# Performance work log

Hardware: AMD Instinct MI355X
Metric: run time of the kernel (lower is better)

The kernel has to match this reference:

```python
import jax, jax.numpy as jnp
import numpy as np

B, H, S, D = 2, 16, 2048, 64
DILATION_RATE = 2

def dilated_global_mask(seq_len: int, dilation_rate: int) -> jnp.ndarray:
    # mask[i, j] = 1 if |i - j| % dilation_rate == 0 else 0  -> [S, S] float32
    i = jnp.arange(seq_len)[:, None]
    j = jnp.arange(seq_len)[None, :]
    return ((jnp.abs(i - j) % dilation_rate) == 0).astype(jnp.float32)

def setup_inputs() -> dict:
    key = jax.random.key(0)
    kq, kk, kv = jax.random.split(key, 3)
    queries = jax.random.normal(kq, (B, H, S, D), dtype=jnp.float32)
    keys = jax.random.normal(kk, (B, H, S, D), dtype=jnp.float32)
    values = jax.random.normal(kv, (B, H, S, D), dtype=jnp.float32)
    return {"queries": queries, "keys": keys, "values": values}

def reference(queries, keys, values):
    depth = queries.shape[-1]
    # scores: [B, H, S, S]
    scores = jnp.einsum("bhqd,bhkd->bhqk", queries, keys)
    scores = scores / jnp.sqrt(jnp.asarray(depth, dtype=jnp.float32))
    gmask = dilated_global_mask(keys.shape[-2], DILATION_RATE)  # [S, S]
    # NOTE: multiplicative masking (masked scores become 0, not -inf), as in source
    masked_scores = scores * gmask
    attention_probs = jax.nn.softmax(masked_scores, axis=-1)
    # dropout is identity at inference (training=None)
    out = jnp.einsum("bhqk,bhkd->bhqd", attention_probs, values)
    return out
```

## Files before the change

### kernel.cpp

```cpp
#include <hip/hip_runtime.h>
#include <hip/hip_bf16.h>


#define B_   2
#define H_   16
#define S_   2048
#define D_   64
#define SP_  1024
#define BQ   128
#define BK   64
#define NKT  (SP_ / BK)
#define NW   4

#define QSCALE 0.180336884f

#if __has_builtin(__builtin_amdgcn_exp2f)
#define EXP2(x) __builtin_amdgcn_exp2f(x)
#else
#define EXP2(x) exp2f(x)
#endif

typedef __bf16 bf16x8 __attribute__((ext_vector_type(8)));
typedef __bf16 bf16x4 __attribute__((ext_vector_type(4)));
typedef float  f32x4  __attribute__((ext_vector_type(4)));
typedef short  s16x4  __attribute__((ext_vector_type(4)));

static __device__ __forceinline__ f32x4 mfma16(bf16x4 a, bf16x4 b, f32x4 c) {
    return __builtin_amdgcn_mfma_f32_16x16x16bf16_1k(
        __builtin_bit_cast(s16x4, a), __builtin_bit_cast(s16x4, b), c, 0, 0, 0);
}

#define KSW(r, c8) ((((c8) ^ ((r) & 7)) << 3))

__global__ __launch_bounds__(256, 2) void attn_kernel(const float* __restrict__ Q,
                                                      const float* __restrict__ K,
                                                      const float* __restrict__ V,
                                                      float* __restrict__ out) {
    const int bh  = blockIdx.x;
    const int par = blockIdx.y;
    const int qt  = blockIdx.z;
    const int tid  = threadIdx.x;
    const int lane = tid & 63;
    const int wave = tid >> 6;
    const int l15  = lane & 15;
    const int quad = lane >> 4;

    __shared__ __align__(16) char arena[33792];
    __bf16 (*kbuf)[BK][64] = (__bf16 (*)[BK][64])arena;
    __bf16 (*vbuf)[D_][64] = (__bf16 (*)[D_][64])(arena + 16384);
    float  (*vred)[64]     = (float  (*)[64])(arena + 32768);

    const size_t base = (size_t)bh * S_ * D_;
    const float* Qb = Q + base;
    const float* Kb = K + base;
    const float* Vb = V + base;
    const int vofs = (par == 0) ? D_ : -D_;

    bf16x8 qf[2][2];
    #pragma unroll
    for (int qt2 = 0; qt2 < 2; ++qt2) {
        const int qrow = qt * BQ + wave * 32 + qt2 * 16 + l15;
        const float* qsrc = Qb + (size_t)(par + 2 * qrow) * D_ + quad * 8;
        #pragma unroll
        for (int ks = 0; ks < 2; ++ks) {
            const float4 a = *(const float4*)(qsrc + ks * 32);
            const float4 b = *(const float4*)(qsrc + ks * 32 + 4);
            bf16x8 w;
            w[0] = (__bf16)(a.x * QSCALE); w[1] = (__bf16)(a.y * QSCALE);
            w[2] = (__bf16)(a.z * QSCALE); w[3] = (__bf16)(a.w * QSCALE);
            w[4] = (__bf16)(b.x * QSCALE); w[5] = (__bf16)(b.y * QSCALE);
            w[6] = (__bf16)(b.z * QSCALE); w[7] = (__bf16)(b.w * QSCALE);
            qf[qt2][ks] = w;
        }
    }

    const int kr0 = tid >> 3;
    const int kc8 = tid & 7;

    float4 pka[2], pkb[2];
    float  pv[16], pvo[16];

    auto issue_loads = [&](int kt) {
        #pragma unroll
        for (int i = 0; i < 2; ++i) {
            const int r = i * 32 + kr0;
            const float* ksrc = Kb + (size_t)(par + 2 * (kt * BK + r)) * D_ + kc8 * 8;
            pka[i] = *(const float4*)ksrc;
            pkb[i] = *(const float4*)(ksrc + 4);
        }
        #pragma unroll
        for (int i = 0; i < 2; ++i) {
            const int c = wave + 4 * i;
            const float* vsrc = Vb + (size_t)(par + 2 * (kt * BK + c * 8)) * D_ + lane;
            #pragma unroll
            for (int j = 0; j < 8; ++j) {
                pv [i * 8 + j] = vsrc[(size_t)(2 * j) * D_];
                pvo[i * 8 + j] = vsrc[(size_t)(2 * j) * D_ + vofs];
            }
        }
    };

    float vo = 0.f;
    auto stage = [&](int buf) {
        #pragma unroll
        for (int i = 0; i < 2; ++i) {
            const int r = i * 32 + kr0;
            bf16x8 w;
            w[0] = (__bf16)pka[i].x; w[1] = (__bf16)pka[i].y;
            w[2] = (__bf16)pka[i].z; w[3] = (__bf16)pka[i].w;
            w[4] = (__bf16)pkb[i].x; w[5] = (__bf16)pkb[i].y;
            w[6] = (__bf16)pkb[i].z; w[7] = (__bf16)pkb[i].w;
            *(bf16x8*)&kbuf[buf][r][KSW(r, kc8)] = w;
        }
        #pragma unroll
        for (int i = 0; i < 2; ++i) {
            const int c = wave + 4 * i;
            bf16x8 w;
            #pragma unroll
            for (int j = 0; j < 8; ++j) w[j] = (__bf16)pv[i * 8 + j];
            *(bf16x8*)&vbuf[buf][lane][KSW(lane, c)] = w;
            vo += ((pvo[i*8+0] + pvo[i*8+1]) + (pvo[i*8+2] + pvo[i*8+3]))
                + ((pvo[i*8+4] + pvo[i*8+5]) + (pvo[i*8+6] + pvo[i*8+7]));
        }
    };

    issue_loads(0);
    stage(0);
    __syncthreads();

    f32x4 acc[2][4];
    #pragma unroll
    for (int q2 = 0; q2 < 2; ++q2)
        #pragma unroll
        for (int dt = 0; dt < 4; ++dt) acc[q2][dt] = (f32x4){0.f, 0.f, 0.f, 0.f};
    float l_acc[2] = {0.f, 0.f};

    for (int kt = 0; kt < NKT; ++kt) {
        const int cur = kt & 1;
        const bool pf = (kt + 1 < NKT);

        if (pf) issue_loads(kt + 1);

        const __bf16 (*kb)[64] = kbuf[cur];
        const __bf16 (*vb)[64] = vbuf[cur];

        bf16x8 ka[2][4];
        #pragma unroll
        for (int ks = 0; ks < 2; ++ks)
            #pragma unroll
            for (int kt4 = 0; kt4 < 4; ++kt4) {
                const int R = kt4 * 16 + l15;
                ka[ks][kt4] = *(const bf16x8*)&kb[R][KSW(R, ks * 4 + quad)];
            }
        bf16x4 va[4][4];
        #pragma unroll
        for (int dt = 0; dt < 4; ++dt) {
            const int R = dt * 16 + l15;
            const int ro = R & 7;
            #pragma unroll
            for (int kt4 = 0; kt4 < 4; ++kt4) {
                const int ch = (kt4 * 2 + (quad >> 1)) ^ ro;
                va[kt4][dt] = *(const bf16x4*)&vb[R][ch * 8 + (quad & 1) * 4];
            }
        }

        #pragma unroll
        for (int qt2 = 0; qt2 < 2; ++qt2) {
            f32x4 st[4];
            #pragma unroll
            for (int kt4 = 0; kt4 < 4; ++kt4) st[kt4] = (f32x4){0.f, 0.f, 0.f, 0.f};
            #pragma unroll
            for (int ks = 0; ks < 2; ++ks)
                #pragma unroll
                for (int kt4 = 0; kt4 < 4; ++kt4)
                    st[kt4] = __builtin_amdgcn_mfma_f32_16x16x32_bf16(
                        ka[ks][kt4], qf[qt2][ks], st[kt4], 0, 0, 0);
            #pragma unroll
            for (int kt4 = 0; kt4 < 4; ++kt4) {
                const float p0 = EXP2(st[kt4][0]);
                const float p1 = EXP2(st[kt4][1]);
                const float p2 = EXP2(st[kt4][2]);
                const float p3 = EXP2(st[kt4][3]);
                l_acc[qt2] += (p0 + p1) + (p2 + p3);
                bf16x4 pb;
                pb[0] = (__bf16)p0; pb[1] = (__bf16)p1;
                pb[2] = (__bf16)p2; pb[3] = (__bf16)p3;
                #pragma unroll
                for (int dt = 0; dt < 4; ++dt)
                    acc[qt2][dt] = mfma16(va[kt4][dt], pb, acc[qt2][dt]);
            }
        }

        if (pf) stage(1 - cur);
        __syncthreads();
    }

    vred[wave][lane] = vo;
    __syncthreads();

    f32x4 vs4[4];
    #pragma unroll
    for (int dt = 0; dt < 4; ++dt) {
        f32x4 s = (f32x4){0.f, 0.f, 0.f, 0.f};
        #pragma unroll
        for (int w = 0; w < NW; ++w)
            s += *(const f32x4*)&vred[w][dt * 16 + quad * 4];
        vs4[dt] = s;
    }
    float rz[2];
    #pragma unroll
    for (int qt2 = 0; qt2 < 2; ++qt2) {
        float Z = l_acc[qt2];
        Z += __shfl_xor(Z, 16);
        Z += __shfl_xor(Z, 32);
        rz[qt2] = 1.0f / (Z + 1024.0f);
    }

    float* tw = (float*)arena + wave * (16 * 68);
    #pragma unroll
    for (int qt2 = 0; qt2 < 2; ++qt2) {
        #pragma unroll
        for (int dt = 0; dt < 4; ++dt) {
            const f32x4 o = (acc[qt2][dt] + vs4[dt]) * rz[qt2];
            *(f32x4*)&tw[l15 * 68 + dt * 16 + quad * 4] = o;
        }
        #pragma unroll
        for (int i = 0; i < 4; ++i) {
            const int q = i * 4 + quad;
            const f32x4 ov = *(const f32x4*)&tw[q * 68 + l15 * 4];
            const int qg = par + 2 * (qt * BQ + wave * 32 + qt2 * 16 + q);
            *(f32x4*)&out[base + (size_t)qg * D_ + l15 * 4] = ov;
        }
    }
}

extern "C" void kernel_launch(void* const* d_in, const int* in_sizes, int n_in,
                              void* d_out, int out_size, void* d_ws, size_t ws_size,
                              hipStream_t stream) {
    const float* Q = (const float*)d_in[0];
    const float* K = (const float*)d_in[1];
    const float* V = (const float*)d_in[2];
    float* out = (float*)d_out;
    attn_kernel<<<dim3(B_ * H_, 2, SP_ / BQ), dim3(256), 0, stream>>>(Q, K, V, out);
}
```

Measured before the change: 112.3 us.

## Split each key tile across two wave groups with LDS reduction of partial outputs

```diff
diff --git a/kernel.cpp b/kernel.cpp
--- a/kernel.cpp
+++ b/kernel.cpp
@@ -10,7 +10,7 @@
 #define BQ   128
 #define BK   64
 #define NKT  (SP_ / BK)
-#define NW   4
+#define NW   8
 
 #define QSCALE 0.180336884f
 
@@ -32,7 +32,7 @@
 
 #define KSW(r, c8) ((((c8) ^ ((r) & 7)) << 3))
 
-__global__ __launch_bounds__(256, 2) void attn_kernel(const float* __restrict__ Q,
+__global__ __launch_bounds__(512, 4) void attn_kernel(const float* __restrict__ Q,
                                                       const float* __restrict__ K,
                                                       const float* __restrict__ V,
                                                       float* __restrict__ out) {
@@ -42,13 +42,17 @@
     const int tid  = threadIdx.x;
     const int lane = tid & 63;
     const int wave = tid >> 6;
+    const int w4   = wave & 3;
+    const int hk   = wave >> 2;
+    const int kt4b = hk * 2;
     const int l15  = lane & 15;
     const int quad = lane >> 4;
 
-    __shared__ __align__(16) char arena[33792];
+    __shared__ __align__(16) char arena[54272];
     __bf16 (*kbuf)[BK][64] = (__bf16 (*)[BK][64])arena;
     __bf16 (*vbuf)[D_][64] = (__bf16 (*)[D_][64])(arena + 16384);
     float  (*vred)[64]     = (float  (*)[64])(arena + 32768);
+    float  (*lred)[2][64]  = (float  (*)[2][64])(arena + 34816);
 
     const size_t base = (size_t)bh * S_ * D_;
     const float* Qb = Q + base;
@@ -59,7 +63,7 @@
     bf16x8 qf[2][2];
     #pragma unroll
     for (int qt2 = 0; qt2 < 2; ++qt2) {
-        const int qrow = qt * BQ + wave * 32 + qt2 * 16 + l15;
+        const int qrow = qt * BQ + w4 * 32 + qt2 * 16 + l15;
         const float* qsrc = Qb + (size_t)(par + 2 * qrow) * D_ + quad * 8;
         #pragma unroll
         for (int ks = 0; ks < 2; ++ks) {
@@ -76,52 +80,37 @@
 
     const int kr0 = tid >> 3;
     const int kc8 = tid & 7;
-
-    float4 pka[2], pkb[2];
-    float  pv[16], pvo[16];
+    const int vc  = wave;
+
+    float4 pka, pkb;
+    float  pv[8], pvo[8];
 
     auto issue_loads = [&](int kt) {
-        #pragma unroll
-        for (int i = 0; i < 2; ++i) {
-            const int r = i * 32 + kr0;
-            const float* ksrc = Kb + (size_t)(par + 2 * (kt * BK + r)) * D_ + kc8 * 8;
-            pka[i] = *(const float4*)ksrc;
-            pkb[i] = *(const float4*)(ksrc + 4);
-        }
-        #pragma unroll
-        for (int i = 0; i < 2; ++i) {
-            const int c = wave + 4 * i;
-            const float* vsrc = Vb + (size_t)(par + 2 * (kt * BK + c * 8)) * D_ + lane;
-            #pragma unroll
-            for (int j = 0; j < 8; ++j) {
-                pv [i * 8 + j] = vsrc[(size_t)(2 * j) * D_];
-                pvo[i * 8 + j] = vsrc[(size_t)(2 * j) * D_ + vofs];
-            }
+        const float* ksrc = Kb + (size_t)(par + 2 * (kt * BK + kr0)) * D_ + kc8 * 8;
+        pka = *(const float4*)ksrc;
+        pkb = *(const float4*)(ksrc + 4);
+        const float* vsrc = Vb + (size_t)(par + 2 * (kt * BK + vc * 8)) * D_ + lane;
+        #pragma unroll
+        for (int j = 0; j < 8; ++j) {
+            pv [j] = vsrc[(size_t)(2 * j) * D_];
+            pvo[j] = vsrc[(size_t)(2 * j) * D_ + vofs];
         }
     };
 
     float vo = 0.f;
     auto stage = [&](int buf) {
-        #pragma unroll
-        for (int i = 0; i < 2; ++i) {
-            const int r = i * 32 + kr0;
-            bf16x8 w;
-            w[0] = (__bf16)pka[i].x; w[1] = (__bf16)pka[i].y;
-            w[2] = (__bf16)pka[i].z; w[3] = (__bf16)pka[i].w;
-            w[4] = (__bf16)pkb[i].x; w[5] = (__bf16)pkb[i].y;
-            w[6] = (__bf16)pkb[i].z; w[7] = (__bf16)pkb[i].w;
-            *(bf16x8*)&kbuf[buf][r][KSW(r, kc8)] = w;
-        }
-        #pragma unroll
-        for (int i = 0; i < 2; ++i) {
-            const int c = wave + 4 * i;
-            bf16x8 w;
-            #pragma unroll
-            for (int j = 0; j < 8; ++j) w[j] = (__bf16)pv[i * 8 + j];
-            *(bf16x8*)&vbuf[buf][lane][KSW(lane, c)] = w;
-            vo += ((pvo[i*8+0] + pvo[i*8+1]) + (pvo[i*8+2] + pvo[i*8+3]))
-                + ((pvo[i*8+4] + pvo[i*8+5]) + (pvo[i*8+6] + pvo[i*8+7]));
-        }
+        bf16x8 w;
+        w[0] = (__bf16)pka.x; w[1] = (__bf16)pka.y;
+        w[2] = (__bf16)pka.z; w[3] = (__bf16)pka.w;
+        w[4] = (__bf16)pkb.x; w[5] = (__bf16)pkb.y;
+        w[6] = (__bf16)pkb.z; w[7] = (__bf16)pkb.w;
+        *(bf16x8*)&kbuf[buf][kr0][KSW(kr0, kc8)] = w;
+        bf16x8 wv;
+        #pragma unroll
+        for (int j = 0; j < 8; ++j) wv[j] = (__bf16)pv[j];
+        *(bf16x8*)&vbuf[buf][lane][KSW(lane, vc)] = wv;
+        vo += ((pvo[0] + pvo[1]) + (pvo[2] + pvo[3]))
+            + ((pvo[4] + pvo[5]) + (pvo[6] + pvo[7]));
     };
 
     issue_loads(0);
@@ -144,50 +133,50 @@
         const __bf16 (*kb)[64] = kbuf[cur];
         const __bf16 (*vb)[64] = vbuf[cur];
 
-        bf16x8 ka[2][4];
+        bf16x8 ka[2][2];
         #pragma unroll
         for (int ks = 0; ks < 2; ++ks)
             #pragma unroll
-            for (int kt4 = 0; kt4 < 4; ++kt4) {
-                const int R = kt4 * 16 + l15;
-                ka[ks][kt4] = *(const bf16x8*)&kb[R][KSW(R, ks * 4 + quad)];
+            for (int t = 0; t < 2; ++t) {
+                const int R = (kt4b + t) * 16 + l15;
+                ka[ks][t] = *(const bf16x8*)&kb[R][KSW(R, ks * 4 + quad)];
             }
-        bf16x4 va[4][4];
+        bf16x4 va[2][4];
         #pragma unroll
         for (int dt = 0; dt < 4; ++dt) {
             const int R = dt * 16 + l15;
             const int ro = R & 7;
             #pragma unroll
-            for (int kt4 = 0; kt4 < 4; ++kt4) {
-                const int ch = (kt4 * 2 + (quad >> 1)) ^ ro;
-                va[kt4][dt] = *(const bf16x4*)&vb[R][ch * 8 + (quad & 1) * 4];
+            for (int t = 0; t < 2; ++t) {
+                const int ch = ((kt4b + t) * 2 + (quad >> 1)) ^ ro;
+                va[t][dt] = *(const bf16x4*)&vb[R][ch * 8 + (quad & 1) * 4];
             }
         }
 
         #pragma unroll
         for (int qt2 = 0; qt2 < 2; ++qt2) {
-            f32x4 st[4];
-            #pragma unroll
-            for (int kt4 = 0; kt4 < 4; ++kt4) st[kt4] = (f32x4){0.f, 0.f, 0.f, 0.f};
+            f32x4 st[2];
+            #pragma unroll
+            for (int t = 0; t < 2; ++t) st[t] = (f32x4){0.f, 0.f, 0.f, 0.f};
             #pragma unroll
             for (int ks = 0; ks < 2; ++ks)
                 #pragma unroll
-                for (int kt4 = 0; kt4 < 4; ++kt4)
-                    st[kt4] = __builtin_amdgcn_mfma_f32_16x16x32_bf16(
-                        ka[ks][kt4], qf[qt2][ks], st[kt4], 0, 0, 0);
-            #pragma unroll
-            for (int kt4 = 0; kt4 < 4; ++kt4) {
-                const float p0 = EXP2(st[kt4][0]);
-                const float p1 = EXP2(st[kt4][1]);
-                const float p2 = EXP2(st[kt4][2]);
-                const float p3 = EXP2(st[kt4][3]);
+                for (int t = 0; t < 2; ++t)
+                    st[t] = __builtin_amdgcn_mfma_f32_16x16x32_bf16(
+                        ka[ks][t], qf[qt2][ks], st[t], 0, 0, 0);
+            #pragma unroll
+            for (int t = 0; t < 2; ++t) {
+                const float p0 = EXP2(st[t][0]);
+                const float p1 = EXP2(st[t][1]);
+                const float p2 = EXP2(st[t][2]);
+                const float p3 = EXP2(st[t][3]);
                 l_acc[qt2] += (p0 + p1) + (p2 + p3);
                 bf16x4 pb;
                 pb[0] = (__bf16)p0; pb[1] = (__bf16)p1;
                 pb[2] = (__bf16)p2; pb[3] = (__bf16)p3;
                 #pragma unroll
                 for (int dt = 0; dt < 4; ++dt)
-                    acc[qt2][dt] = mfma16(va[kt4][dt], pb, acc[qt2][dt]);
+                    acc[qt2][dt] = mfma16(va[t][dt], pb, acc[qt2][dt]);
             }
         }
 
@@ -196,39 +185,59 @@
     }
 
     vred[wave][lane] = vo;
-    __syncthreads();
-
-    f32x4 vs4[4];
-    #pragma unroll
-    for (int dt = 0; dt < 4; ++dt) {
-        f32x4 s = (f32x4){0.f, 0.f, 0.f, 0.f};
-        #pragma unroll
-        for (int w = 0; w < NW; ++w)
-            s += *(const f32x4*)&vred[w][dt * 16 + quad * 4];
-        vs4[dt] = s;
-    }
-    float rz[2];
+
+    float lf[2];
     #pragma unroll
     for (int qt2 = 0; qt2 < 2; ++qt2) {
         float Z = l_acc[qt2];
         Z += __shfl_xor(Z, 16);
         Z += __shfl_xor(Z, 32);
-        rz[qt2] = 1.0f / (Z + 1024.0f);
-    }
-
-    float* tw = (float*)arena + wave * (16 * 68);
+        lf[qt2] = Z;
+    }
+
+    if (hk) {
+        f32x4* ad = (f32x4*)(arena + (size_t)w4 * 8192);
+        #pragma unroll
+        for (int qt2 = 0; qt2 < 2; ++qt2) {
+            lred[w4][qt2][lane] = lf[qt2];
+            #pragma unroll
+            for (int dt = 0; dt < 4; ++dt)
+                ad[(qt2 * 4 + dt) * 64 + lane] = acc[qt2][dt];
+        }
+    }
+    __syncthreads();
+    if (hk) return;
+
+    f32x4 vs4[4];
+    #pragma unroll
+    for (int dt = 0; dt < 4; ++dt) {
+        f32x4 s = (f32x4){0.f, 0.f, 0.f, 0.f};
+        #pragma unroll
+        for (int w = 0; w < NW; ++w)
+            s += *(const f32x4*)&vred[w][dt * 16 + quad * 4];
+        vs4[dt] = s;
+    }
+    float rz[2];
+    #pragma unroll
+    for (int qt2 = 0; qt2 < 2; ++qt2)
+        rz[qt2] = 1.0f / (lf[qt2] + lred[w4][qt2][lane] + 1024.0f);
+
+    const f32x4* ad = (const f32x4*)(arena + (size_t)w4 * 8192);
+
+    float* tw = (float*)(arena + 36864) + w4 * (16 * 68);
     #pragma unroll
     for (int qt2 = 0; qt2 < 2; ++qt2) {
         #pragma unroll
         for (int dt = 0; dt < 4; ++dt) {
-            const f32x4 o = (acc[qt2][dt] + vs4[dt]) * rz[qt2];
+            const f32x4 o = (acc[qt2][dt] + ad[(qt2 * 4 + dt) * 64 + lane] + vs4[dt])
+                          * rz[qt2];
             *(f32x4*)&tw[l15 * 68 + dt * 16 + quad * 4] = o;
         }
         #pragma unroll
         for (int i = 0; i < 4; ++i) {
             const int q = i * 4 + quad;
             const f32x4 ov = *(const f32x4*)&tw[q * 68 + l15 * 4];
-            const int qg = par + 2 * (qt * BQ + wave * 32 + qt2 * 16 + q);
+            const int qg = par + 2 * (qt * BQ + w4 * 32 + qt2 * 16 + q);
             *(f32x4*)&out[base + (size_t)qg * D_ + l15 * 4] = ov;
         }
     }
@@ -241,5 +250,5 @@
     const float* K = (const float*)d_in[1];
     const float* V = (const float*)d_in[2];
     float* out = (float*)d_out;
-    attn_kernel<<<dim3(B_ * H_, 2, SP_ / BQ), dim3(256), 0, stream>>>(Q, K, V, out);
+    attn_kernel<<<dim3(B_ * H_, 2, SP_ / BQ), dim3(512), 0, stream>>>(Q, K, V, out);
 }
```

Measured after the change: 119.6 us. 6.5% more time.

## Precompute off-parity V column sums in a separate kernel and halve query tile

Applied to the files above, without the earlier changes.

```diff
diff --git a/kernel.cpp b/kernel.cpp
--- a/kernel.cpp
+++ b/kernel.cpp
@@ -7,10 +7,9 @@
 #define S_   2048
 #define D_   64
 #define SP_  1024
-#define BQ   128
+#define BQ   64
 #define BK   64
 #define NKT  (SP_ / BK)
-#define NW   4
 
 #define QSCALE 0.180336884f
 
@@ -32,9 +31,32 @@
 
 #define KSW(r, c8) ((((c8) ^ ((r) & 7)) << 3))
 
-__global__ __launch_bounds__(256, 2) void attn_kernel(const float* __restrict__ Q,
+__global__ __launch_bounds__(1024) void vsum_kernel(const float* __restrict__ V,
+                                                    float* __restrict__ vs) {
+    const int bp  = blockIdx.x;
+    const int bh  = bp >> 1;
+    const int par = bp & 1;
+    const int d   = threadIdx.x & 63;
+    const int rg  = threadIdx.x >> 6;
+    const float* Vb = V + (size_t)bh * S_ * D_;
+    float s = 0.f;
+    for (int r = rg; r < SP_; r += 16)
+        s += Vb[(size_t)(par + 2 * r) * D_ + d];
+    __shared__ float red[16][64];
+    red[rg][d] = s;
+    __syncthreads();
+    if (rg == 0) {
+        float t = 0.f;
+        #pragma unroll
+        for (int i = 0; i < 16; ++i) t += red[i][d];
+        vs[(size_t)bp * 64 + d] = t;
+    }
+}
+
+__global__ __launch_bounds__(256, 4) void attn_kernel(const float* __restrict__ Q,
                                                       const float* __restrict__ K,
                                                       const float* __restrict__ V,
+                                                      const float* __restrict__ vs,
                                                       float* __restrict__ out) {
     const int bh  = blockIdx.x;
     const int par = blockIdx.y;
@@ -45,21 +67,18 @@
     const int l15  = lane & 15;
     const int quad = lane >> 4;
 
-    __shared__ __align__(16) char arena[33792];
+    __shared__ __align__(16) char arena[32768];
     __bf16 (*kbuf)[BK][64] = (__bf16 (*)[BK][64])arena;
     __bf16 (*vbuf)[D_][64] = (__bf16 (*)[D_][64])(arena + 16384);
-    float  (*vred)[64]     = (float  (*)[64])(arena + 32768);
 
     const size_t base = (size_t)bh * S_ * D_;
     const float* Qb = Q + base;
     const float* Kb = K + base;
     const float* Vb = V + base;
-    const int vofs = (par == 0) ? D_ : -D_;
-
-    bf16x8 qf[2][2];
-    #pragma unroll
-    for (int qt2 = 0; qt2 < 2; ++qt2) {
-        const int qrow = qt * BQ + wave * 32 + qt2 * 16 + l15;
+
+    bf16x8 qf[2];
+    {
+        const int qrow = qt * BQ + wave * 16 + l15;
         const float* qsrc = Qb + (size_t)(par + 2 * qrow) * D_ + quad * 8;
         #pragma unroll
         for (int ks = 0; ks < 2; ++ks) {
@@ -70,7 +89,7 @@
             w[2] = (__bf16)(a.z * QSCALE); w[3] = (__bf16)(a.w * QSCALE);
             w[4] = (__bf16)(b.x * QSCALE); w[5] = (__bf16)(b.y * QSCALE);
             w[6] = (__bf16)(b.z * QSCALE); w[7] = (__bf16)(b.w * QSCALE);
-            qf[qt2][ks] = w;
+            qf[ks] = w;
         }
     }
 
@@ -78,7 +97,7 @@
     const int kc8 = tid & 7;
 
     float4 pka[2], pkb[2];
-    float  pv[16], pvo[16];
+    float  pv[16];
 
     auto issue_loads = [&](int kt) {
         #pragma unroll
@@ -93,14 +112,11 @@
             const int c = wave + 4 * i;
             const float* vsrc = Vb + (size_t)(par + 2 * (kt * BK + c * 8)) * D_ + lane;
             #pragma unroll
-            for (int j = 0; j < 8; ++j) {
-                pv [i * 8 + j] = vsrc[(size_t)(2 * j) * D_];
-                pvo[i * 8 + j] = vsrc[(size_t)(2 * j) * D_ + vofs];
-            }
+            for (int j = 0; j < 8; ++j)
+                pv[i * 8 + j] = vsrc[(size_t)(2 * j) * D_];
         }
     };
 
-    float vo = 0.f;
     auto stage = [&](int buf) {
         #pragma unroll
         for (int i = 0; i < 2; ++i) {
@@ -119,8 +135,6 @@
             #pragma unroll
             for (int j = 0; j < 8; ++j) w[j] = (__bf16)pv[i * 8 + j];
             *(bf16x8*)&vbuf[buf][lane][KSW(lane, c)] = w;
-            vo += ((pvo[i*8+0] + pvo[i*8+1]) + (pvo[i*8+2] + pvo[i*8+3]))
-                + ((pvo[i*8+4] + pvo[i*8+5]) + (pvo[i*8+6] + pvo[i*8+7]));
         }
     };
 
@@ -128,12 +142,10 @@
     stage(0);
     __syncthreads();
 
-    f32x4 acc[2][4];
+    f32x4 acc[4];
     #pragma unroll
-    for (int q2 = 0; q2 < 2; ++q2)
-        #pragma unroll
-        for (int dt = 0; dt < 4; ++dt) acc[q2][dt] = (f32x4){0.f, 0.f, 0.f, 0.f};
-    float l_acc[2] = {0.f, 0.f};
+    for (int dt = 0; dt < 4; ++dt) acc[dt] = (f32x4){0.f, 0.f, 0.f, 0.f};
+    float l_acc = 0.f;
 
     for (int kt = 0; kt < NKT; ++kt) {
         const int cur = kt & 1;
@@ -164,73 +176,54 @@
             }
         }
 
-        #pragma unroll
-        for (int qt2 = 0; qt2 < 2; ++qt2) {
-            f32x4 st[4];
-            #pragma unroll
-            for (int kt4 = 0; kt4 < 4; ++kt4) st[kt4] = (f32x4){0.f, 0.f, 0.f, 0.f};
-            #pragma unroll
-            for (int ks = 0; ks < 2; ++ks)
-                #pragma unroll
-                for (int kt4 = 0; kt4 < 4; ++kt4)
-                    st[kt4] = __builtin_amdgcn_mfma_f32_16x16x32_bf16(
-                        ka[ks][kt4], qf[qt2][ks], st[kt4], 0, 0, 0);
-            #pragma unroll
-            for (int kt4 = 0; kt4 < 4; ++kt4) {
-                const float p0 = EXP2(st[kt4][0]);
-                const float p1 = EXP2(st[kt4][1]);
-                const float p2 = EXP2(st[kt4][2]);
-                const float p3 = EXP2(st[kt4][3]);
-                l_acc[qt2] += (p0 + p1) + (p2 + p3);
-                bf16x4 pb;
-                pb[0] = (__bf16)p0; pb[1] = (__bf16)p1;
-                pb[2] = (__bf16)p2; pb[3] = (__bf16)p3;
-                #pragma unroll
-                for (int dt = 0; dt < 4; ++dt)
-                    acc[qt2][dt] = mfma16(va[kt4][dt], pb, acc[qt2][dt]);
-            }
+        f32x4 st[4];
+        #pragma unroll
+        for (int kt4 = 0; kt4 < 4; ++kt4) st[kt4] = (f32x4){0.f, 0.f, 0.f, 0.f};
+        #pragma unroll
+        for (int ks = 0; ks < 2; ++ks)
+            #pragma unroll
+            for (int kt4 = 0; kt4 < 4; ++kt4)
+                st[kt4] = __builtin_amdgcn_mfma_f32_16x16x32_bf16(
+                    ka[ks][kt4], qf[ks], st[kt4], 0, 0, 0);
+        #pragma unroll
+        for (int kt4 = 0; kt4 < 4; ++kt4) {
+            const float p0 = EXP2(st[kt4][0]);
+            const float p1 = EXP2(st[kt4][1]);
+            const float p2 = EXP2(st[kt4][2]);
+            const float p3 = EXP2(st[kt4][3]);
+            l_acc += (p0 + p1) + (p2 + p3);
+            bf16x4 pb;
+            pb[0] = (__bf16)p0; pb[1] = (__bf16)p1;
+            pb[2] = (__bf16)p2; pb[3] = (__bf16)p3;
+            #pragma unroll
+            for (int dt = 0; dt < 4; ++dt)
+                acc[dt] = mfma16(va[kt4][dt], pb, acc[dt]);
         }
 
         if (pf) stage(1 - cur);
         __syncthreads();
     }
 
-    vred[wave][lane] = vo;
-    __syncthreads();
-
-    f32x4 vs4[4];
+    float Z = l_acc;
+    Z += __shfl_xor(Z, 16);
+    Z += __shfl_xor(Z, 32);
+    const float rz = 1.0f / (Z + 1024.0f);
+
+    const float* vso = vs + ((size_t)(bh * 2 + (1 - par))) * 64;
+
+    float* tw = (float*)arena + wave * (16 * 68);
     #pragma unroll
     for (int dt = 0; dt < 4; ++dt) {
-        f32x4 s = (f32x4){0.f, 0.f, 0.f, 0.f};
-        #pragma unroll
-        for (int w = 0; w < NW; ++w)
-            s += *(const f32x4*)&vred[w][dt * 16 + quad * 4];
-        vs4[dt] = s;
-    }
-    float rz[2];
+        const f32x4 vs4 = *(const f32x4*)&vso[dt * 16 + quad * 4];
+        const f32x4 o = (acc[dt] + vs4) * rz;
+        *(f32x4*)&tw[l15 * 68 + dt * 16 + quad * 4] = o;
+    }
     #pragma unroll
-    for (int qt2 = 0; qt2 < 2; ++qt2) {
-        float Z = l_acc[qt2];
-        Z += __shfl_xor(Z, 16);
-        Z += __shfl_xor(Z, 32);
-        rz[qt2] = 1.0f / (Z + 1024.0f);
-    }
-
-    float* tw = (float*)arena + wave * (16 * 68);
-    #pragma unroll
-    for (int qt2 = 0; qt2 < 2; ++qt2) {
-        #pragma unroll
-        for (int dt = 0; dt < 4; ++dt) {
-            const f32x4 o = (acc[qt2][dt] + vs4[dt]) * rz[qt2];
-            *(f32x4*)&tw[l15 * 68 + dt * 16 + quad * 4] = o;
-        }
-        #pragma unroll
-        for (int i = 0; i < 4; ++i) {
-            const int q = i * 4 + quad;
-            const f32x4 ov = *(const f32x4*)&tw[q * 68 + l15 * 4];
-            const int qg = par + 2 * (qt * BQ + wave * 32 + qt2 * 16 + q);
-            *(f32x4*)&out[base + (size_t)qg * D_ + l15 * 4] = ov;
-        }
+    for (int i = 0; i < 4; ++i) {
+        const int q = i * 4 + quad;
+        const f32x4 ov = *(const f32x4*)&tw[q * 68 + l15 * 4];
+        const int qg = par + 2 * (qt * BQ + wave * 16 + q);
+        *(f32x4*)&out[base + (size_t)qg * D_ + l15 * 4] = ov;
     }
 }
 
@@ -241,5 +234,7 @@
     const float* K = (const float*)d_in[1];
     const float* V = (const float*)d_in[2];
     float* out = (float*)d_out;
-    attn_kernel<<<dim3(B_ * H_, 2, SP_ / BQ), dim3(256), 0, stream>>>(Q, K, V, out);
-}
+    float* vs = (float*)d_ws;
+    vsum_kernel<<<dim3(B_ * H_ * 2), dim3(1024), 0, stream>>>(V, vs);
+    attn_kernel<<<dim3(B_ * H_, 2, SP_ / BQ), dim3(256), 0, stream>>>(Q, K, V, vs, out);
+}
```

Result: slower. 134.5 us (+19.8%).
